# Kernel tuning notes

Measured on AMD Instinct MI355X. Metric: run time of the kernel, lower is better.

## Reference

```python
import jax, jax.numpy as jnp
import numpy as np

N = 100000
E = 1600000
CIN = 32
COUT = 32
K = 5
EPS = 1e-15      # PyG GMMConv EPS in sigma^2 denominator
BN_EPS = 1e-5    # torch BatchNorm1d default eps


def gmm_conv(x, edge_index, edge_attr, g, mu, sigma, root, bias):
    """PyG GMMConv (MoNet), aggr='mean', root_weight=True, bias=True."""
    src, dst = edge_index[0], edge_index[1]
    n = x.shape[0]
    k = mu.shape[0]
    cout = root.shape[1]
    xg = (x @ g).reshape(n, k, cout)                # [N, K, out]
    xj = xg[src]                                    # gather: [E, K, out]
    d = edge_attr[:, None, :] - mu[None, :, :]      # [E, K, 3]
    w = jnp.exp(-0.5 * jnp.sum(d * d / (EPS + sigma[None] ** 2), axis=-1))  # [E, K]
    msg = jnp.einsum('eko,ek->eo', xj, w)           # [E, out]
    agg = jax.ops.segment_sum(msg, dst, num_segments=n)
    cnt = jax.ops.segment_sum(jnp.ones((msg.shape[0],), x.dtype), dst, num_segments=n)
    agg = agg / jnp.clip(cnt, 1.0)[:, None]         # mean aggregation
    return agg + x @ root + bias


def batch_norm(x, gamma, beta):
    # training-mode BatchNorm1d: biased batch statistics over node dim
    m = x.mean(0)
    v = x.var(0)
    return (x - m) * jax.lax.rsqrt(v + BN_EPS) * gamma + beta


def setup_inputs() -> dict:
    key = jax.random.key(0)
    ks = jax.random.split(key, 12)
    p = lambda k, s, sc=0.1: jax.random.normal(k, s, jnp.float32) * sc
    return {
        'x': jax.random.normal(ks[0], (N, CIN), jnp.float32),
        'edge_index': jax.random.randint(ks[1], (2, E), 0, N, jnp.int32),
        'edge_attr': jax.random.uniform(ks[2], (E, 3), jnp.float32),
        # left conv1: in -> out, K=5
        'g1': p(ks[3], (CIN, K * COUT)), 'mu1': p(ks[4], (K, 3), 1.0), 'sigma1': jnp.ones((K, 3), jnp.float32),
        'root1': p(ks[5], (CIN, COUT)), 'b1': jnp.zeros((COUT,), jnp.float32),
        'gam1': jnp.ones((COUT,), jnp.float32), 'bet1': jnp.zeros((COUT,), jnp.float32),
        # left conv2: out -> out, K=5
        'g2': p(ks[6], (COUT, K * COUT)), 'mu2': p(ks[7], (K, 3), 1.0), 'sigma2': jnp.ones((K, 3), jnp.float32),
        'root2': p(ks[8], (COUT, COUT)), 'b2': jnp.zeros((COUT,), jnp.float32),
        'gam2': jnp.ones((COUT,), jnp.float32), 'bet2': jnp.zeros((COUT,), jnp.float32),
        # shortcut conv: in -> out, K=1
        'gs': p(ks[9], (CIN, 1 * COUT)), 'mus': p(ks[10], (1, 3), 1.0), 'sigmas': jnp.ones((1, 3), jnp.float32),
        'roots': p(ks[11], (CIN, COUT)), 'bs': jnp.zeros((COUT,), jnp.float32),
        'gams': jnp.ones((COUT,), jnp.float32), 'bets': jnp.zeros((COUT,), jnp.float32),
    }


def reference(x, edge_index, edge_attr,
              g1, mu1, sigma1, root1, b1, gam1, bet1,
              g2, mu2, sigma2, root2, b2, gam2, bet2,
              gs, mus, sigmas, roots, bs, gams, bets):
    h = jax.nn.elu(batch_norm(gmm_conv(x, edge_index, edge_attr, g1, mu1, sigma1, root1, b1), gam1, bet1))
    h = batch_norm(gmm_conv(h, edge_index, edge_attr, g2, mu2, sigma2, root2, b2), gam2, bet2)
    s = batch_norm(gmm_conv(x, edge_index, edge_attr, gs, mus, sigmas, roots, bs), gams, bets)
    return jax.nn.elu(h + s)
```

## Files before the change

kernel.cpp:

```cpp
#include <hip/hip_runtime.h>
#include <hip/hip_bf16.h>
#include <math.h>


#define ELU(v) ((v) > 0.f ? (v) : (__expf(v) - 1.f))

using short8  = __attribute__((ext_vector_type(8))) short;
using floatx4 = __attribute__((ext_vector_type(4))) float;

__device__ inline ushort f2bf(float f) {
    __hip_bfloat16 h = __float2bfloat16(f);
    return *reinterpret_cast<ushort*>(&h);
}
__device__ inline float bflo(unsigned u) { return __uint_as_float(u << 16); }
__device__ inline float bfhi(unsigned u) { return __uint_as_float(u & 0xffff0000u); }
__device__ inline unsigned pack_bf2(float lo, float hi) {
    return ((unsigned)f2bf(hi) << 16) | (unsigned)f2bf(lo);
}

__global__ __launch_bounds__(256) void prep_xb(
    const float* __restrict__ x, unsigned* __restrict__ XB, int N)
{
    const int idx = blockIdx.x * blockDim.x + threadIdx.x;
    if (idx >= N * 16) return;
    const float2 p = ((const float2*)x)[idx];
    XB[idx] = pack_bf2(p.x, p.y);
}

__global__ __launch_bounds__(256) void prep_hxb(
    const float* __restrict__ out1, const float* __restrict__ coef,
    unsigned* __restrict__ XB, int N)
{
    const int idx = blockIdx.x * blockDim.x + threadIdx.x;
    if (idx >= N * 16) return;
    const int l = idx & 15;
    const float2 p = ((const float2*)out1)[idx];
    const int c0 = 2 * l, c1 = 2 * l + 1;
    float v0 = p.x * coef[c0] + coef[32 + c0];
    float v1 = p.y * coef[c1] + coef[32 + c1];
    v0 = ELU(v0); v1 = ELU(v1);
    XB[idx] = pack_bf2(v0, v1);
}

#define CH 4096
__global__ __launch_bounds__(256) void binfill_k(
    const int* __restrict__ ei, const float* __restrict__ attr,
    int* __restrict__ gcur, unsigned long long* __restrict__ pay0,
    int E, int NB, int CAPc)
{
    __shared__ unsigned long long srec[CH];
    __shared__ unsigned char sbin[CH];
    __shared__ int cnt[256], offs[256], wcur[256], gbase[256], sc[256];

    const int t = threadIdx.x;
    const int e0 = blockIdx.x * CH;
    const int nrec = min(CH, E - e0);

    cnt[t] = 0;
    __syncthreads();

    unsigned long long rec[16];
    int bin[16];
#pragma unroll
    for (int r = 0; r < 16; ++r) {
        const int e = e0 + r * 256 + t;
        bin[r] = -1;
        if (e < E) {
            const int s = ei[e], d = ei[E + e];
            const float a0 = attr[(size_t)e * 3 + 0];
            const float a1 = attr[(size_t)e * 3 + 1];
            const float a2 = attr[(size_t)e * 3 + 2];
            const unsigned q0 = (unsigned)min(max((int)(a0 * 4096.f), 0), 4095);
            const unsigned q1 = (unsigned)min(max((int)(a1 * 4096.f), 0), 4095);
            const unsigned q2 = (unsigned)min(max((int)(a2 * 4096.f), 0), 4095);
            rec[r] = (unsigned long long)(unsigned)s
                   | ((unsigned long long)(d & 511) << 17)
                   | ((unsigned long long)q0 << 26)
                   | ((unsigned long long)q1 << 38)
                   | ((unsigned long long)q2 << 50);
            bin[r] = d >> 9;
            atomicAdd(&cnt[bin[r]], 1);
        }
    }
    __syncthreads();

    const int v = cnt[t];
    sc[t] = v;
    __syncthreads();
    for (int o = 1; o < 256; o <<= 1) {
        const int xx = (t >= o) ? sc[t - o] : 0;
        __syncthreads();
        sc[t] += xx;
        __syncthreads();
    }
    offs[t] = sc[t] - v;
    wcur[t] = sc[t] - v;
    __syncthreads();

#pragma unroll
    for (int r = 0; r < 16; ++r) {
        if (bin[r] >= 0) {
            const int pos = atomicAdd(&wcur[bin[r]], 1);
            srec[pos] = rec[r];
            sbin[pos] = (unsigned char)bin[r];
        }
    }
    __syncthreads();

    if (t < NB && cnt[t] > 0) gbase[t] = atomicAdd(&gcur[t], cnt[t]);
    __syncthreads();

    for (int i = t; i < nrec; i += 256) {
        const int b = sbin[i];
        const int idx = gbase[b] + (i - offs[b]);
        if (idx < CAPc)
            pay0[(size_t)b * CAPc + idx] = srec[i];
    }
}

__global__ void bucket_scan(const int* __restrict__ gcur, int* __restrict__ bbase,
                            int NB)
{
    __shared__ int sh[256];
    const int t = threadIdx.x;
    const int v = (t < NB) ? gcur[t] : 0;
    sh[t] = v;
    __syncthreads();
    for (int o = 1; o < 256; o <<= 1) {
        const int xx = (t >= o) ? sh[t - o] : 0;
        __syncthreads();
        sh[t] += xx;
        __syncthreads();
    }
    if (t < NB) bbase[t] = sh[t] - v;
}

__global__ __launch_bounds__(256) void scatter2_k(
    const unsigned long long* __restrict__ pay0, const int* __restrict__ gcur,
    const int* __restrict__ bbase, int* __restrict__ row_ptr,
    unsigned long long* __restrict__ pay, int N, int CAPc, int NB)
{
    const int b = blockIdx.x;
    const int t = threadIdx.x;
    const int d0 = b << 9;
    const int nd = min(512, N - d0);

    __shared__ int cnt[512];
    __shared__ int offs[512];
    __shared__ int sscan[256];

    for (int i = t; i < 512; i += 256) cnt[i] = 0;
    __syncthreads();

    const int total = min(gcur[b], CAPc);
    const unsigned long long* src = pay0 + (size_t)b * CAPc;

    for (int i = t; i < total; i += 256) {
        const int dlo = (int)((src[i] >> 17) & 511);
        atomicAdd(&cnt[dlo], 1);
    }
    __syncthreads();

    const int c0 = cnt[2 * t], c1 = cnt[2 * t + 1];
    const int pairsum = c0 + c1;
    sscan[t] = pairsum;
    __syncthreads();
    for (int o = 1; o < 256; o <<= 1) {
        const int xx = (t >= o) ? sscan[t - o] : 0;
        __syncthreads();
        sscan[t] += xx;
        __syncthreads();
    }
    const int excl = sscan[t] - pairsum;
    offs[2 * t] = excl;
    offs[2 * t + 1] = excl + c0;
    __syncthreads();
    const int btotal = sscan[255];

    const int base = bbase[b];
    for (int i = t; i < nd; i += 256) row_ptr[d0 + i] = base + offs[i];
    if (b == NB - 1 && t == 0) row_ptr[N] = base + btotal;

    for (int i = t; i < 512; i += 256) cnt[i] = offs[i];
    __syncthreads();

    for (int i = t; i < total; i += 256) {
        const unsigned long long rec = src[i];
        const int dlo = (int)((rec >> 17) & 511);
        const int p = atomicAdd(&cnt[dlo], 1);
        pay[base + p] = rec;
    }
}

template <bool HAS_S>
__global__ __launch_bounds__(256) void gt_k(
    const unsigned* __restrict__ XB,
    const unsigned long long* __restrict__ payload,
    const int* __restrict__ row_ptr,
    const float* __restrict__ mu_m, const float* __restrict__ sg_m,
    const float* __restrict__ mu_s, const float* __restrict__ sg_s,
    const float* __restrict__ g,
    const float* __restrict__ rootm,
    const float* __restrict__ bm,
    const float* __restrict__ gss,
    const float* __restrict__ rootss,
    const float* __restrict__ bss,
    float* __restrict__ out_m, float* __restrict__ out_s,
    float* __restrict__ stats_m, float* __restrict__ stats_s,
    int N)
{
    constexpr int KS = HAS_S ? 6 : 5;
    constexpr int SLS = KS + 1;
    constexpr int STRIDE = SLS * 16 + 4;
    constexpr float DQ = 1.0f / 4096.0f;

    __shared__ float wbuf[16][17][8];
    __shared__ unsigned sA[16 * STRIDE];
    __shared__ float sred[128];

    const int tid = threadIdx.x;
    const int l = tid & 15, grp = tid >> 4;
    const int lane = tid & 63, l4 = lane & 15, quad = lane >> 4;
    const int wv = tid >> 6;
    const int half = wv & 1;

    if (tid < 128) sred[tid] = 0.f;

    const bool convRole = (wv < 2);
    const bool sRole = HAS_S && (wv >= 2);
    short8 Bf[6];
    float bias0 = 0.f;
    if (convRole) {
#pragma unroll
        for (int s = 0; s < 5; ++s)
#pragma unroll
            for (int j = 0; j < 8; ++j)
                Bf[s][j] = (short)f2bf(g[(quad * 8 + j) * 160 + s * 32 + 16 * half + l4]);
#pragma unroll
        for (int j = 0; j < 8; ++j)
            Bf[5][j] = (short)f2bf(rootm[(quad * 8 + j) * 32 + 16 * half + l4]);
        bias0 = bm[16 * half + l4];
    } else if (sRole) {
#pragma unroll
        for (int j = 0; j < 8; ++j) {
            Bf[0][j] = (short)f2bf(gss[(quad * 8 + j) * 32 + 16 * half + l4]);
            Bf[1][j] = (short)f2bf(rootss[(quad * 8 + j) * 32 + 16 * half + l4]);
        }
        bias0 = bss[16 * half + l4];
    }

    float mm[15], im[15];
#pragma unroll
    for (int i = 0; i < 15; ++i) {
        mm[i] = mu_m[i];
        float s = sg_m[i];
        im[i] = 1.0f / (1e-15f + s * s);
    }
    float ms[3], is[3];
    if (HAS_S) {
#pragma unroll
        for (int i = 0; i < 3; ++i) {
            ms[i] = mu_s[i];
            float s = sg_s[i];
            is[i] = 1.0f / (1e-15f + s * s);
        }
    }

    const int dst = blockIdx.x * 16 + grp;
    float2 acc[KS];
#pragma unroll
    for (int k = 0; k < KS; ++k) acc[k] = make_float2(0.f, 0.f);

    int rp0 = 0, deg = 0;
    if (dst < N) { rp0 = row_ptr[dst]; deg = row_ptr[dst + 1] - rp0; }

    auto body = [&](int j) {
        const float4 a = *(const float4*)&wbuf[grp][j][0];
        const float4 b = *(const float4*)&wbuf[grp][j][4];
        const int sj = __float_as_int(a.x);
        const unsigned u = XB[(size_t)sj * 16 + l];
        const float x0 = bflo(u), x1 = bfhi(u);
        acc[0].x = fmaf(a.y, x0, acc[0].x); acc[0].y = fmaf(a.y, x1, acc[0].y);
        acc[1].x = fmaf(a.z, x0, acc[1].x); acc[1].y = fmaf(a.z, x1, acc[1].y);
        acc[2].x = fmaf(a.w, x0, acc[2].x); acc[2].y = fmaf(a.w, x1, acc[2].y);
        acc[3].x = fmaf(b.x, x0, acc[3].x); acc[3].y = fmaf(b.x, x1, acc[3].y);
        acc[4].x = fmaf(b.y, x0, acc[4].x); acc[4].y = fmaf(b.y, x1, acc[4].y);
        if (HAS_S) {
            acc[5].x = fmaf(b.z, x0, acc[5].x); acc[5].y = fmaf(b.z, x1, acc[5].y);
        }
    };

    for (int base = 0; base < deg; base += 16) {
        const int nj = min(16, deg - base);
        if (l < nj) {
            unsigned long long pq = payload[rp0 + base + l];
            const int src = (int)(pq & 0x1FFFFull);
            float p0 = ((int)((pq >> 26) & 0xFFF) + 0.5f) * DQ;
            float p1 = ((int)((pq >> 38) & 0xFFF) + 0.5f) * DQ;
            float p2 = ((int)((pq >> 50) & 0xFFF) + 0.5f) * DQ;
            float w[5], wS = 0.f;
#pragma unroll
            for (int k = 0; k < 5; ++k) {
                float d0 = p0 - mm[k * 3 + 0];
                float d1 = p1 - mm[k * 3 + 1];
                float d2 = p2 - mm[k * 3 + 2];
                float q = d0 * d0 * im[k * 3 + 0] + d1 * d1 * im[k * 3 + 1]
                        + d2 * d2 * im[k * 3 + 2];
                w[k] = __expf(-0.5f * q);
            }
            if (HAS_S) {
                float d0 = p0 - ms[0], d1 = p1 - ms[1], d2 = p2 - ms[2];
                float q = d0 * d0 * is[0] + d1 * d1 * is[1] + d2 * d2 * is[2];
                wS = __expf(-0.5f * q);
            }
            float4* wp = (float4*)&wbuf[grp][l][0];
            wp[0] = make_float4(__int_as_float(src), w[0], w[1], w[2]);
            wp[1] = make_float4(w[3], w[4], wS, 0.f);
        }
        int j = 0;
        for (; j + 3 < nj; j += 4) { body(j); body(j + 1); body(j + 2); body(j + 3); }
        for (; j < nj; ++j) body(j);
    }

    {
        unsigned* arow = sA + grp * STRIDE;
        const float invd = 1.0f / fmaxf((float)deg, 1.0f);
        const bool ok = (dst < N);
#pragma unroll
        for (int k = 0; k < KS; ++k)
            arow[k * 16 + l] = ok ? pack_bf2(acc[k].x * invd, acc[k].y * invd) : 0u;
        arow[KS * 16 + l] = ok ? XB[(size_t)dst * 16 + l] : 0u;
    }
    __syncthreads();

    if (convRole || sRole) {
        floatx4 C = {0.f, 0.f, 0.f, 0.f};
        if (convRole) {
#pragma unroll
            for (int s = 0; s < 6; ++s) {
                const int slot = (s < 5) ? s : KS;
                const uint4 av = *(const uint4*)(sA + l4 * STRIDE + slot * 16 + quad * 4);
                const short8 A = *reinterpret_cast<const short8*>(&av);
                C = __builtin_amdgcn_mfma_f32_16x16x32_bf16(A, Bf[s], C, 0, 0, 0);
            }
        } else {
#pragma unroll
            for (int s = 0; s < 2; ++s) {
                const int slot = 5 + s;
                const uint4 av = *(const uint4*)(sA + l4 * STRIDE + slot * 16 + quad * 4);
                const short8 A = *reinterpret_cast<const short8*>(&av);
                C = __builtin_amdgcn_mfma_f32_16x16x32_bf16(A, Bf[s], C, 0, 0, 0);
            }
        }

        float* outp = convRole ? out_m : out_s;
        float ps = 0.f, pq = 0.f;
#pragma unroll
        for (int r = 0; r < 4; ++r) {
            const int n = blockIdx.x * 16 + quad * 4 + r;
            if (n < N) {
                const float v = C[r] + bias0;
                outp[(size_t)n * 32 + 16 * half + l4] = v;
                ps += v; pq += v * v;
            }
        }
        const int base = convRole ? 0 : 64;
        atomicAdd(&sred[base + 16 * half + l4], ps);
        atomicAdd(&sred[base + 32 + 16 * half + l4], pq);
    }
    __syncthreads();

    const int spread = (blockIdx.x & 7) * 64;
    if (tid < 64) atomicAdd(&stats_m[spread + tid], sred[tid]);
    else if (HAS_S && tid < 128) atomicAdd(&stats_s[spread + tid - 64], sred[tid]);
}

__global__ void coef_k(const float* __restrict__ stats, const float* __restrict__ gam,
                       const float* __restrict__ bet, float* __restrict__ coef,
                       float invN)
{
    int c = threadIdx.x;
    if (c < 32) {
        float s = 0.f, q = 0.f;
        for (int p = 0; p < 8; ++p) { s += stats[p * 64 + c]; q += stats[p * 64 + 32 + c]; }
        float m = s * invN;
        float v = fmaxf(q * invN - m * m, 0.f);
        float sc = gam[c] * rsqrtf(v + 1e-5f);
        coef[c] = sc;
        coef[32 + c] = bet[c] - m * sc;
    }
}

__global__ __launch_bounds__(256) void final_k(
    const float* __restrict__ o2, const float* __restrict__ os,
    const float* __restrict__ c2, const float* __restrict__ cs,
    float* __restrict__ out, int total)
{
    int idx = blockIdx.x * blockDim.x + threadIdx.x;
    if (idx >= total) return;
    int c = idx & 31;
    float v = o2[idx] * c2[c] + c2[32 + c] + os[idx] * cs[c] + cs[32 + c];
    out[idx] = ELU(v);
}

extern "C" void kernel_launch(void* const* d_in, const int* in_sizes, int n_in,
                              void* d_out, int out_size, void* d_ws, size_t ws_size,
                              hipStream_t stream)
{
    const float* x      = (const float*)d_in[0];
    const int*   ei     = (const int*)d_in[1];
    const float* attr   = (const float*)d_in[2];
    const float* g1     = (const float*)d_in[3];
    const float* mu1    = (const float*)d_in[4];
    const float* sig1   = (const float*)d_in[5];
    const float* root1  = (const float*)d_in[6];
    const float* b1     = (const float*)d_in[7];
    const float* gam1   = (const float*)d_in[8];
    const float* bet1   = (const float*)d_in[9];
    const float* g2     = (const float*)d_in[10];
    const float* mu2    = (const float*)d_in[11];
    const float* sig2   = (const float*)d_in[12];
    const float* root2  = (const float*)d_in[13];
    const float* b2     = (const float*)d_in[14];
    const float* gam2   = (const float*)d_in[15];
    const float* bet2   = (const float*)d_in[16];
    const float* gs     = (const float*)d_in[17];
    const float* mus    = (const float*)d_in[18];
    const float* sigs   = (const float*)d_in[19];
    const float* roots  = (const float*)d_in[20];
    const float* bs     = (const float*)d_in[21];
    const float* gams   = (const float*)d_in[22];
    const float* bets   = (const float*)d_in[23];

    const int N = in_sizes[0] / 32;
    const int E = in_sizes[1] / 2;
    const int total = N * 32;
    const int ntiles = (N + 15) / 16;
    const int NB = (N + 511) >> 9;
    const int CAPc = ((((E + NB - 1) / NB) * 5) / 4 + 15) & ~15;

    char* ws = (char*)d_ws;
    size_t off = 0;
    auto carve = [&](size_t bytes) {
        void* p = ws + off;
        off = (off + bytes + 255) & ~(size_t)255;
        return p;
    };
    unsigned* XB   = (unsigned*)carve((size_t)N * 16 * 4);
    float*  OUT1   = (float*)carve((size_t)N * 32 * 4);
    float*  OUT2   = (float*)carve((size_t)N * 32 * 4);
    float*  OUTS   = (float*)carve((size_t)N * 32 * 4);
    unsigned long long* PAY  = (unsigned long long*)carve((size_t)E * 8);
    unsigned long long* PAY0 = (unsigned long long*)carve((size_t)NB * CAPc * 8);
    int*    ROWP   = (int*)carve((size_t)(N + 1) * 4);
    int*    GCUR   = (int*)carve(512 * 4);
    int*    BBASE  = GCUR + 256;
    float*  STATS  = (float*)carve(3 * 512 * 4);
    float*  COEF   = (float*)carve(3 * 64 * 4);
    float* stats1 = STATS, *stats2 = STATS + 512, *statsS = STATS + 1024;
    float* coef1 = COEF, *coef2 = COEF + 64, *coefS = COEF + 128;
    (void)ws_size; (void)n_in; (void)out_size;

    const float invN = 1.0f / (float)N;
    const int ew = (total + 255) / 256;
    const int epb = (N * 16 + 255) / 256;
    const int nfb = (E + CH - 1) / CH;

    hipMemsetAsync(GCUR, 0, 256 * 4, stream);
    hipMemsetAsync(STATS, 0, 3 * 512 * 4, stream);

    binfill_k<<<nfb, 256, 0, stream>>>(ei, attr, GCUR, PAY0, E, NB, CAPc);
    bucket_scan<<<1, 256, 0, stream>>>(GCUR, BBASE, NB);
    scatter2_k<<<NB, 256, 0, stream>>>(PAY0, GCUR, BBASE, ROWP, PAY, N, CAPc, NB);

    prep_xb<<<epb, 256, 0, stream>>>(x, XB, N);
    gt_k<true><<<ntiles, 256, 0, stream>>>(XB, PAY, ROWP,
        mu1, sig1, mus, sigs, g1, root1, b1, gs, roots, bs,
        OUT1, OUTS, stats1, statsS, N);
    coef_k<<<1, 64, 0, stream>>>(stats1, gam1, bet1, coef1, invN);
    coef_k<<<1, 64, 0, stream>>>(statsS, gams, bets, coefS, invN);

    prep_hxb<<<epb, 256, 0, stream>>>(OUT1, coef1, XB, N);
    gt_k<false><<<ntiles, 256, 0, stream>>>(XB, PAY, ROWP,
        mu2, sig2, nullptr, nullptr, g2, root2, b2, nullptr, nullptr, nullptr,
        OUT2, nullptr, stats2, nullptr, N);
    coef_k<<<1, 64, 0, stream>>>(stats2, gam2, bet2, coef2, invN);

    final_k<<<ew, 256, 0, stream>>>(OUT2, OUTS, coef2, coefS, (float*)d_out, total);
}
```

Before: 326.4 us.

## Make gather-transform kernel persistent and fold small scan/coef launches

The gather-transform kernel becomes grid-strided over 16-node tiles with a grid capped at 2048 blocks. Weight fragments and mu/sigma constants are now loaded once per block, and batch-norm partial sums are reduced once per block instead of once per tile. The separate bucket prefix-scan kernel is removed; each scatter block instead reduces the preceding bucket counts itself. The two coefficient kernels are merged into a single launch. Together these cut launch count, per-tile setup and global stat atomics, at the cost of less parallel slack for load balancing across irregular node degrees.

Measured after the change: 324.2 us. No clear change (-0.7%).

```diff
diff --git a/kernel.cpp b/kernel.cpp
--- a/kernel.cpp
+++ b/kernel.cpp
@@ -118,27 +118,10 @@
     }
 }
 
-__global__ void bucket_scan(const int* __restrict__ gcur, int* __restrict__ bbase,
-                            int NB)
-{
-    __shared__ int sh[256];
-    const int t = threadIdx.x;
-    const int v = (t < NB) ? gcur[t] : 0;
-    sh[t] = v;
-    __syncthreads();
-    for (int o = 1; o < 256; o <<= 1) {
-        const int xx = (t >= o) ? sh[t - o] : 0;
-        __syncthreads();
-        sh[t] += xx;
-        __syncthreads();
-    }
-    if (t < NB) bbase[t] = sh[t] - v;
-}
-
 __global__ __launch_bounds__(256) void scatter2_k(
     const unsigned long long* __restrict__ pay0, const int* __restrict__ gcur,
-    const int* __restrict__ bbase, int* __restrict__ row_ptr,
-    unsigned long long* __restrict__ pay, int N, int CAPc, int NB)
+    int* __restrict__ row_ptr, unsigned long long* __restrict__ pay,
+    int N, int CAPc, int NB)
 {
     const int b = blockIdx.x;
     const int t = threadIdx.x;
@@ -148,9 +131,16 @@
     __shared__ int cnt[512];
     __shared__ int offs[512];
     __shared__ int sscan[256];
-
+    __shared__ int ssum[256];
+
+    ssum[t] = (t < b && t < NB) ? gcur[t] : 0;
     for (int i = t; i < 512; i += 256) cnt[i] = 0;
     __syncthreads();
+    for (int o = 128; o > 0; o >>= 1) {
+        if (t < o) ssum[t] += ssum[t + o];
+        __syncthreads();
+    }
+    const int base = ssum[0];
 
     const int total = min(gcur[b], CAPc);
     const unsigned long long* src = pay0 + (size_t)b * CAPc;
@@ -177,7 +167,6 @@
     __syncthreads();
     const int btotal = sscan[255];
 
-    const int base = bbase[b];
     for (int i = t; i < nd; i += 256) row_ptr[d0 + i] = base + offs[i];
     if (b == NB - 1 && t == 0) row_ptr[N] = base + btotal;
 
@@ -207,7 +196,7 @@
     const float* __restrict__ bss,
     float* __restrict__ out_m, float* __restrict__ out_s,
     float* __restrict__ stats_m, float* __restrict__ stats_s,
-    int N)
+    int N, int ntiles)
 {
     constexpr int KS = HAS_S ? 6 : 5;
     constexpr int SLS = KS + 1;
@@ -224,8 +213,6 @@
     const int wv = tid >> 6;
     const int half = wv & 1;
 
-    if (tid < 128) sred[tid] = 0.f;
-
     const bool convRole = (wv < 2);
     const bool sRole = HAS_S && (wv >= 2);
     short8 Bf[6];
@@ -266,129 +253,147 @@
         }
     }
 
-    const int dst = blockIdx.x * 16 + grp;
-    float2 acc[KS];
-#pragma unroll
-    for (int k = 0; k < KS; ++k) acc[k] = make_float2(0.f, 0.f);
-
-    int rp0 = 0, deg = 0;
-    if (dst < N) { rp0 = row_ptr[dst]; deg = row_ptr[dst + 1] - rp0; }
-
-    auto body = [&](int j) {
-        const float4 a = *(const float4*)&wbuf[grp][j][0];
-        const float4 b = *(const float4*)&wbuf[grp][j][4];
-        const int sj = __float_as_int(a.x);
-        const unsigned u = XB[(size_t)sj * 16 + l];
-        const float x0 = bflo(u), x1 = bfhi(u);
-        acc[0].x = fmaf(a.y, x0, acc[0].x); acc[0].y = fmaf(a.y, x1, acc[0].y);
-        acc[1].x = fmaf(a.z, x0, acc[1].x); acc[1].y = fmaf(a.z, x1, acc[1].y);
-        acc[2].x = fmaf(a.w, x0, acc[2].x); acc[2].y = fmaf(a.w, x1, acc[2].y);
-        acc[3].x = fmaf(b.x, x0, acc[3].x); acc[3].y = fmaf(b.x, x1, acc[3].y);
-        acc[4].x = fmaf(b.y, x0, acc[4].x); acc[4].y = fmaf(b.y, x1, acc[4].y);
-        if (HAS_S) {
-            acc[5].x = fmaf(b.z, x0, acc[5].x); acc[5].y = fmaf(b.z, x1, acc[5].y);
-        }
-    };
-
-    for (int base = 0; base < deg; base += 16) {
-        const int nj = min(16, deg - base);
-        if (l < nj) {
-            unsigned long long pq = payload[rp0 + base + l];
-            const int src = (int)(pq & 0x1FFFFull);
-            float p0 = ((int)((pq >> 26) & 0xFFF) + 0.5f) * DQ;
-            float p1 = ((int)((pq >> 38) & 0xFFF) + 0.5f) * DQ;
-            float p2 = ((int)((pq >> 50) & 0xFFF) + 0.5f) * DQ;
-            float w[5], wS = 0.f;
-#pragma unroll
-            for (int k = 0; k < 5; ++k) {
-                float d0 = p0 - mm[k * 3 + 0];
-                float d1 = p1 - mm[k * 3 + 1];
-                float d2 = p2 - mm[k * 3 + 2];
-                float q = d0 * d0 * im[k * 3 + 0] + d1 * d1 * im[k * 3 + 1]
-                        + d2 * d2 * im[k * 3 + 2];
-                w[k] = __expf(-0.5f * q);
+    float ps = 0.f, pq = 0.f;
+
+    for (int tile = blockIdx.x; tile < ntiles; tile += gridDim.x) {
+        const int dst = tile * 16 + grp;
+        float2 acc[KS];
+#pragma unroll
+        for (int k = 0; k < KS; ++k) acc[k] = make_float2(0.f, 0.f);
+
+        int rp0 = 0, deg = 0;
+        if (dst < N) { rp0 = row_ptr[dst]; deg = row_ptr[dst + 1] - rp0; }
+
+        auto body = [&](int j) {
+            const float4 a = *(const float4*)&wbuf[grp][j][0];
+            const float4 b = *(const float4*)&wbuf[grp][j][4];
+            const int sj = __float_as_int(a.x);
+            const unsigned u = XB[(size_t)sj * 16 + l];
+            const float x0 = bflo(u), x1 = bfhi(u);
+            acc[0].x = fmaf(a.y, x0, acc[0].x); acc[0].y = fmaf(a.y, x1, acc[0].y);
+            acc[1].x = fmaf(a.z, x0, acc[1].x); acc[1].y = fmaf(a.z, x1, acc[1].y);
+            acc[2].x = fmaf(a.w, x0, acc[2].x); acc[2].y = fmaf(a.w, x1, acc[2].y);
+            acc[3].x = fmaf(b.x, x0, acc[3].x); acc[3].y = fmaf(b.x, x1, acc[3].y);
+            acc[4].x = fmaf(b.y, x0, acc[4].x); acc[4].y = fmaf(b.y, x1, acc[4].y);
+            if (HAS_S) {
+                acc[5].x = fmaf(b.z, x0, acc[5].x); acc[5].y = fmaf(b.z, x1, acc[5].y);
             }
-            if (HAS_S) {
-                float d0 = p0 - ms[0], d1 = p1 - ms[1], d2 = p2 - ms[2];
-                float q = d0 * d0 * is[0] + d1 * d1 * is[1] + d2 * d2 * is[2];
-                wS = __expf(-0.5f * q);
+        };
+
+        for (int base = 0; base < deg; base += 16) {
+            const int nj = min(16, deg - base);
+            if (l < nj) {
+                unsigned long long pq8 = payload[rp0 + base + l];
+                const int src = (int)(pq8 & 0x1FFFFull);
+                float p0 = ((int)((pq8 >> 26) & 0xFFF) + 0.5f) * DQ;
+                float p1 = ((int)((pq8 >> 38) & 0xFFF) + 0.5f) * DQ;
+                float p2 = ((int)((pq8 >> 50) & 0xFFF) + 0.5f) * DQ;
+                float w[5], wS = 0.f;
+#pragma unroll
+                for (int k = 0; k < 5; ++k) {
+                    float d0 = p0 - mm[k * 3 + 0];
+                    float d1 = p1 - mm[k * 3 + 1];
+                    float d2 = p2 - mm[k * 3 + 2];
+                    float q = d0 * d0 * im[k * 3 + 0] + d1 * d1 * im[k * 3 + 1]
+                            + d2 * d2 * im[k * 3 + 2];
+                    w[k] = __expf(-0.5f * q);
+                }
+                if (HAS_S) {
+                    float d0 = p0 - ms[0], d1 = p1 - ms[1], d2 = p2 - ms[2];
+                    float q = d0 * d0 * is[0] + d1 * d1 * is[1] + d2 * d2 * is[2];
+                    wS = __expf(-0.5f * q);
+                }
+                float4* wp = (float4*)&wbuf[grp][l][0];
+                wp[0] = make_float4(__int_as_float(src), w[0], w[1], w[2]);
+                wp[1] = make_float4(w[3], w[4], wS, 0.f);
             }
-            float4* wp = (float4*)&wbuf[grp][l][0];
-            wp[0] = make_float4(__int_as_float(src), w[0], w[1], w[2]);
-            wp[1] = make_float4(w[3], w[4], wS, 0.f);
-        }
-        int j = 0;
-        for (; j + 3 < nj; j += 4) { body(j); body(j + 1); body(j + 2); body(j + 3); }
-        for (; j < nj; ++j) body(j);
-    }
-
-    {
-        unsigned* arow = sA + grp * STRIDE;
-        const float invd = 1.0f / fmaxf((float)deg, 1.0f);
-        const bool ok = (dst < N);
-#pragma unroll
-        for (int k = 0; k < KS; ++k)
-            arow[k * 16 + l] = ok ? pack_bf2(acc[k].x * invd, acc[k].y * invd) : 0u;
-        arow[KS * 16 + l] = ok ? XB[(size_t)dst * 16 + l] : 0u;
-    }
-    __syncthreads();
-
-    if (convRole || sRole) {
-        floatx4 C = {0.f, 0.f, 0.f, 0.f};
-        if (convRole) {
-#pragma unroll
-            for (int s = 0; s < 6; ++s) {
-                const int slot = (s < 5) ? s : KS;
-                const uint4 av = *(const uint4*)(sA + l4 * STRIDE + slot * 16 + quad * 4);
-                const short8 A = *reinterpret_cast<const short8*>(&av);
-                C = __builtin_amdgcn_mfma_f32_16x16x32_bf16(A, Bf[s], C, 0, 0, 0);
+            int j = 0;
+            for (; j + 3 < nj; j += 4) { body(j); body(j + 1); body(j + 2); body(j + 3); }
+            for (; j < nj; ++j) body(j);
+        }
+
+        {
+            unsigned* arow = sA + grp * STRIDE;
+            const float invd = 1.0f / fmaxf((float)deg, 1.0f);
+            const bool ok = (dst < N);
+#pragma unroll
+            for (int k = 0; k < KS; ++k)
+                arow[k * 16 + l] = ok ? pack_bf2(acc[k].x * invd, acc[k].y * invd) : 0u;
+            arow[KS * 16 + l] = ok ? XB[(size_t)dst * 16 + l] : 0u;
+        }
+        __syncthreads();
+
+        if (convRole || sRole) {
+            floatx4 C = {0.f, 0.f, 0.f, 0.f};
+            if (convRole) {
+#pragma unroll
+                for (int s = 0; s < 6; ++s) {
+                    const int slot = (s < 5) ? s : KS;
+                    const uint4 av = *(const uint4*)(sA + l4 * STRIDE + slot * 16 + quad * 4);
+                    const short8 A = *reinterpret_cast<const short8*>(&av);
+                    C = __builtin_amdgcn_mfma_f32_16x16x32_bf16(A, Bf[s], C, 0, 0, 0);
+                }
+            } else {
+#pragma unroll
+                for (int s = 0; s < 2; ++s) {
+                    const int slot = 5 + s;
+                    const uint4 av = *(const uint4*)(sA + l4 * STRIDE + slot * 16 + quad * 4);
+                    const short8 A = *reinterpret_cast<const short8*>(&av);
+                    C = __builtin_amdgcn_mfma_f32_16x16x32_bf16(A, Bf[s], C, 0, 0, 0);
+                }
             }
-        } else {
-#pragma unroll
-            for (int s = 0; s < 2; ++s) {
-                const int slot = 5 + s;
-                const uint4 av = *(const uint4*)(sA + l4 * STRIDE + slot * 16 + quad * 4);
-                const short8 A = *reinterpret_cast<const short8*>(&av);
-                C = __builtin_amdgcn_mfma_f32_16x16x32_bf16(A, Bf[s], C, 0, 0, 0);
+
+            float* outp = convRole ? out_m : out_s;
+#pragma unroll
+            for (int r = 0; r < 4; ++r) {
+                const int n = tile * 16 + quad * 4 + r;
+                if (n < N) {
+                    const float v = C[r] + bias0;
+                    outp[(size_t)n * 32 + 16 * half + l4] = v;
+                    ps += v; pq += v * v;
+                }
             }
         }
-
-        float* outp = convRole ? out_m : out_s;
-        float ps = 0.f, pq = 0.f;
-#pragma unroll
-        for (int r = 0; r < 4; ++r) {
-            const int n = blockIdx.x * 16 + quad * 4 + r;
-            if (n < N) {
-                const float v = C[r] + bias0;
-                outp[(size_t)n * 32 + 16 * half + l4] = v;
-                ps += v; pq += v * v;
-            }
-        }
-        const int base = convRole ? 0 : 64;
-        atomicAdd(&sred[base + 16 * half + l4], ps);
-        atomicAdd(&sred[base + 32 + 16 * half + l4], pq);
-    }
-    __syncthreads();
-
+        __syncthreads();
+    }
+
+    if (tid < 128) sred[tid] = 0.f;
+    __syncthreads();
+    if (convRole) {
+        atomicAdd(&sred[16 * half + l4], ps);
+        atomicAdd(&sred[32 + 16 * half + l4], pq);
+    } else if (sRole) {
+        atomicAdd(&sred[64 + 16 * half + l4], ps);
+        atomicAdd(&sred[96 + 16 * half + l4], pq);
+    }
+    __syncthreads();
     const int spread = (blockIdx.x & 7) * 64;
     if (tid < 64) atomicAdd(&stats_m[spread + tid], sred[tid]);
     else if (HAS_S && tid < 128) atomicAdd(&stats_s[spread + tid - 64], sred[tid]);
 }
 
-__global__ void coef_k(const float* __restrict__ stats, const float* __restrict__ gam,
-                       const float* __restrict__ bet, float* __restrict__ coef,
-                       float invN)
-{
-    int c = threadIdx.x;
-    if (c < 32) {
-        float s = 0.f, q = 0.f;
-        for (int p = 0; p < 8; ++p) { s += stats[p * 64 + c]; q += stats[p * 64 + 32 + c]; }
-        float m = s * invN;
-        float v = fmaxf(q * invN - m * m, 0.f);
-        float sc = gam[c] * rsqrtf(v + 1e-5f);
-        coef[c] = sc;
-        coef[32 + c] = bet[c] - m * sc;
-    }
+__global__ void coef2_k(const float* __restrict__ stats1, const float* __restrict__ gam1,
+                        const float* __restrict__ bet1, float* __restrict__ coef1,
+                        const float* __restrict__ stats2, const float* __restrict__ gam2,
+                        const float* __restrict__ bet2, float* __restrict__ coef2,
+                        float invN)
+{
+    const int t = threadIdx.x;
+    const int set = t >> 6;
+    const int c = t & 63;
+    if (c >= 32) return;
+    const float* stats = set ? stats2 : stats1;
+    const float* gam = set ? gam2 : gam1;
+    const float* bet = set ? bet2 : bet1;
+    float* coef = set ? coef2 : coef1;
+    if (set && !stats) return;
+    float s = 0.f, q = 0.f;
+    for (int p = 0; p < 8; ++p) { s += stats[p * 64 + c]; q += stats[p * 64 + 32 + c]; }
+    float m = s * invN;
+    float v = fmaxf(q * invN - m * m, 0.f);
+    float sc = gam[c] * rsqrtf(v + 1e-5f);
+    coef[c] = sc;
+    coef[32 + c] = bet[c] - m * sc;
 }
 
 __global__ __launch_bounds__(256) void final_k(
@@ -453,8 +458,7 @@
     unsigned long long* PAY  = (unsigned long long*)carve((size_t)E * 8);
     unsigned long long* PAY0 = (unsigned long long*)carve((size_t)NB * CAPc * 8);
     int*    ROWP   = (int*)carve((size_t)(N + 1) * 4);
-    int*    GCUR   = (int*)carve(512 * 4);
-    int*    BBASE  = GCUR + 256;
+    int*    GCUR   = (int*)carve(256 * 4);
     float*  STATS  = (float*)carve(3 * 512 * 4);
     float*  COEF   = (float*)carve(3 * 64 * 4);
     float* stats1 = STATS, *stats2 = STATS + 512, *statsS = STATS + 1024;
@@ -465,26 +469,27 @@
     const int ew = (total + 255) / 256;
     const int epb = (N * 16 + 255) / 256;
     const int nfb = (E + CH - 1) / CH;
+    const int gtb = ntiles < 2048 ? ntiles : 2048;
 
     hipMemsetAsync(GCUR, 0, 256 * 4, stream);
     hipMemsetAsync(STATS, 0, 3 * 512 * 4, stream);
 
     binfill_k<<<nfb, 256, 0, stream>>>(ei, attr, GCUR, PAY0, E, NB, CAPc);
-    bucket_scan<<<1, 256, 0, stream>>>(GCUR, BBASE, NB);
-    scatter2_k<<<NB, 256, 0, stream>>>(PAY0, GCUR, BBASE, ROWP, PAY, N, CAPc, NB);
+    scatter2_k<<<NB, 256, 0, stream>>>(PAY0, GCUR, ROWP, PAY, N, CAPc, NB);
 
     prep_xb<<<epb, 256, 0, stream>>>(x, XB, N);
-    gt_k<true><<<ntiles, 256, 0, stream>>>(XB, PAY, ROWP,
+    gt_k<true><<<gtb, 256, 0, stream>>>(XB, PAY, ROWP,
         mu1, sig1, mus, sigs, g1, root1, b1, gs, roots, bs,
-        OUT1, OUTS, stats1, statsS, N);
-    coef_k<<<1, 64, 0, stream>>>(stats1, gam1, bet1, coef1, invN);
-    coef_k<<<1, 64, 0, stream>>>(statsS, gams, bets, coefS, invN);
+        OUT1, OUTS, stats1, statsS, N, ntiles);
+    coef2_k<<<1, 128, 0, stream>>>(stats1, gam1, bet1, coef1,
+                                   statsS, gams, bets, coefS, invN);
 
     prep_hxb<<<epb, 256, 0, stream>>>(OUT1, coef1, XB, N);
-    gt_k<false><<<ntiles, 256, 0, stream>>>(XB, PAY, ROWP,
+    gt_k<false><<<gtb, 256, 0, stream>>>(XB, PAY, ROWP,
         mu2, sig2, nullptr, nullptr, g2, root2, b2, nullptr, nullptr, nullptr,
-        OUT2, nullptr, stats2, nullptr, N);
-    coef_k<<<1, 64, 0, stream>>>(stats2, gam2, bet2, coef2, invN);
+        OUT2, nullptr, stats2, nullptr, N, ntiles);
+    coef2_k<<<1, 128, 0, stream>>>(stats2, gam2, bet2, coef2,
+                                   nullptr, nullptr, nullptr, nullptr, invN);
 
     final_k<<<ew, 256, 0, stream>>>(OUT2, OUTS, coef2, coefS, (float*)d_out, total);
 }
```
